# Performance work log

Measured on AMD Instinct MI355X. Metric: run time of the kernel, lower is better.

The kernel has to match this reference:

```python
import jax, jax.numpy as jnp
import numpy as np

B, S, D, H = 2, 2048, 1024, 16
DK = D // H


def setup_inputs() -> dict:
    key = jax.random.key(0)
    ks = jax.random.split(key, 11)
    inp = {
        'query': jax.random.normal(ks[0], (B, S, D), jnp.float32),
        'key':   jax.random.normal(ks[1], (B, S, D), jnp.float32),
        'value': jax.random.normal(ks[2], (B, S, D), jnp.float32),
        # causal mask, broadcast over heads like mask.unsqueeze(1)
        'mask': jnp.broadcast_to(jnp.tril(jnp.ones((S, S), jnp.int32)), (B, S, S)),
    }
    s = 1.0 / np.sqrt(D)
    for i, nm in enumerate(['q', 'k', 'v', 'o']):
        inp[f'W{nm}'] = jax.random.normal(ks[3 + i], (D, D), jnp.float32) * s
        inp[f'b{nm}'] = jnp.zeros((D,), jnp.float32)
    return inp


def reference(query, key, value, mask, Wq, bq, Wk, bk, Wv, bv, Wo, bo):
    def proj(x, W, b):
        # [B,S,D] -> [B,H,S,DK]
        y = x @ W.T + b
        return y.reshape(B, S, H, DK).transpose(0, 2, 1, 3)

    q = proj(query, Wq, bq)
    k = proj(key, Wk, bk)
    v = proj(value, Wv, bv)

    scores = jnp.einsum('bhsd,bhtd->bhst', q, k) / np.sqrt(DK)
    scores = jnp.where(mask[:, None, :, :] == 0, -1e9, scores)
    p = jax.nn.softmax(scores, axis=-1)  # dropout in eval mode = identity
    x = jnp.einsum('bhst,bhtd->bhsd', p, v)
    x = x.transpose(0, 2, 1, 3).reshape(B, S, D)
    return x @ Wo.T + bo
```

## Files before the change

### kernel.cpp

```cpp
#include <hip/hip_runtime.h>
#include <stdint.h>

#define BB 2
#define SS 2048
#define DD 1024
#define HH 16
#define DKK 64
#define EE 4194304
#define WEE 1048576
#define QSCALE 0.1803368801f

typedef __attribute__((ext_vector_type(8))) short bf16x8;
typedef __attribute__((ext_vector_type(4))) float f32x4;
typedef __attribute__((ext_vector_type(4))) unsigned short u16x4;

__device__ __forceinline__ unsigned short f2bf(float f) {
    union { float f; unsigned int i; } c; c.f = f;
    unsigned int u = c.i;
    return (unsigned short)((u + 0x7FFFu + ((u >> 16) & 1u)) >> 16);
}
__device__ __forceinline__ float bf2f(unsigned short u) {
    union { float f; unsigned int i; } c; c.i = ((unsigned int)u) << 16; return c.f;
}
__device__ __forceinline__ float load1f(const void* p, int idx, int isbf) {
    return isbf ? bf2f(((const unsigned short*)p)[idx]) : ((const float*)p)[idx];
}

#define GLDS16(gp, lp)                                                              \
    __builtin_amdgcn_global_load_lds(                                               \
        (const __attribute__((address_space(1))) void*)(gp),                        \
        (__attribute__((address_space(3))) void*)(lp), 16, 0, 0)

__global__ void detect_dtype_k(const unsigned short* __restrict__ q,
                               int* __restrict__ flag) {
    const int lane = threadIdx.x;
    unsigned short u = q[lane * 2];
    int ex = (u >> 7) & 0xFF;
    bool bad = (ex != 0) && (ex < 110 || ex > 137);
    unsigned long long m = __ballot(bad);
    if (lane == 0) *flag = (__popcll(m) >= 8) ? 0 : 1;
}

__global__ __launch_bounds__(256)
void convert_k(const float* __restrict__ q, const float* __restrict__ k,
               const float* __restrict__ v,
               const float* __restrict__ wq, const float* __restrict__ wk,
               const float* __restrict__ wv, const float* __restrict__ wo,
               unsigned short* __restrict__ Xc, unsigned short* __restrict__ Wc,
               const int* __restrict__ flagp)
{
    if (*flagp) return;
    const size_t e = ((size_t)blockIdx.x * 256 + threadIdx.x) * 8;
    const float* src; unsigned short* dst; size_t off;
    if (e < (size_t)3 * EE) {
        const int t = (int)(e / EE);
        src = (t == 0) ? q : (t == 1) ? k : v;
        off = e - (size_t)t * EE;
        dst = Xc + (size_t)t * EE;
    } else {
        const size_t we = e - (size_t)3 * EE;
        const int t = (int)(we >> 20);
        src = (t == 0) ? wq : (t == 1) ? wk : (t == 2) ? wv : wo;
        off = we & (WEE - 1);
        dst = Wc + (size_t)t * WEE;
    }
    const float4 a = *(const float4*)(src + off);
    const float4 b = *(const float4*)(src + off + 4);
    bf16x8 o;
    o[0] = (short)f2bf(a.x); o[1] = (short)f2bf(a.y);
    o[2] = (short)f2bf(a.z); o[3] = (short)f2bf(a.w);
    o[4] = (short)f2bf(b.x); o[5] = (short)f2bf(b.y);
    o[6] = (short)f2bf(b.z); o[7] = (short)f2bf(b.w);
    *(bf16x8*)(dst + off) = o;
}

__global__ __launch_bounds__(256)
void gemm_qkv(const void* __restrict__ Xq, const void* __restrict__ Xk,
              const void* __restrict__ Xv,
              const void* __restrict__ Wqp, const void* __restrict__ Wkp,
              const void* __restrict__ Wvp,
              const void* __restrict__ bqp, const void* __restrict__ bkp,
              const void* __restrict__ bvp,
              const unsigned short* __restrict__ Xc,
              const unsigned short* __restrict__ Wc,
              unsigned short* __restrict__ qb, unsigned short* __restrict__ kb,
              unsigned short* __restrict__ vtb, const int* __restrict__ flagp)
{
    const int isbf = *flagp;
    const int z = blockIdx.z;
    const unsigned short* Xg = isbf
        ? (const unsigned short*)((z == 0) ? Xq : (z == 1) ? Xk : Xv)
        : Xc + (size_t)z * EE;
    const unsigned short* Wg = isbf
        ? (const unsigned short*)((z == 0) ? Wqp : (z == 1) ? Wkp : Wvp)
        : Wc + (size_t)z * WEE;
    const void* bias = (z == 0) ? bqp : (z == 1) ? bkp : bvp;

    __shared__ __align__(16) unsigned short As[2][128 * 32];
    __shared__ __align__(16) unsigned short Bs[2][128 * 32];

    const int tid  = threadIdx.x;
    const int lane = tid & 63, w = tid >> 6;
    const int l15  = lane & 15, quad = lane >> 4;
    const int wr = (w >> 1) * 64, wc = (w & 1) * 64;
    const int r0 = blockIdx.x * 128, c0 = blockIdx.y * 128;
    const int srow = tid >> 2, scol = (tid & 3) << 3;

    const unsigned short* xp0 = Xg + (size_t)(r0 + srow) * DD + scol;
    const unsigned short* xp1 = Xg + (size_t)(r0 + 64 + srow) * DD + scol;
    const unsigned short* wp0 = Wg + (size_t)(c0 + srow) * DD + scol;
    const unsigned short* wp1 = Wg + (size_t)(c0 + 64 + srow) * DD + scol;

#define STAGE_QKV(buf, kk)                                                     \
    do {                                                                       \
        GLDS16(xp0 + (kk), &As[buf][tid * 8]);                                 \
        GLDS16(xp1 + (kk), &As[buf][2048 + tid * 8]);                          \
        GLDS16(wp0 + (kk), &Bs[buf][tid * 8]);                                 \
        GLDS16(wp1 + (kk), &Bs[buf][2048 + tid * 8]);                          \
    } while (0)

#define COMPUTE_QKV(buf)                                                       \
    do {                                                                       \
        bf16x8 af[4], bfr[4];                                                  \
        _Pragma("unroll")                                                      \
        for (int mi = 0; mi < 4; ++mi)                                         \
            af[mi] = *(const bf16x8*)(&As[buf][(wr + mi * 16 + l15) * 32 +     \
                                               quad * 8]);                     \
        _Pragma("unroll")                                                      \
        for (int ni = 0; ni < 4; ++ni)                                         \
            bfr[ni] = *(const bf16x8*)(&Bs[buf][(wc + ni * 16 + l15) * 32 +    \
                                                quad * 8]);                    \
        _Pragma("unroll")                                                      \
        for (int mi = 0; mi < 4; ++mi)                                         \
            _Pragma("unroll")                                                  \
            for (int ni = 0; ni < 4; ++ni)                                     \
                acc[mi][ni] = __builtin_amdgcn_mfma_f32_16x16x32_bf16(         \
                    af[mi], bfr[ni], acc[mi][ni], 0, 0, 0);                    \
    } while (0)

    f32x4 acc[4][4] = {};

    STAGE_QKV(0, 0);
    asm volatile("s_waitcnt vmcnt(0)" ::: "memory");
    __builtin_amdgcn_s_barrier();
    __builtin_amdgcn_sched_barrier(0);

    int cur = 0;
    for (int k0 = 0; k0 < DD - 32; k0 += 32) {
        STAGE_QKV(cur ^ 1, k0 + 32);
        __builtin_amdgcn_sched_barrier(0);
        COMPUTE_QKV(cur);
        asm volatile("s_waitcnt vmcnt(0)" ::: "memory");
        __builtin_amdgcn_s_barrier();
        __builtin_amdgcn_sched_barrier(0);
        cur ^= 1;
    }
    COMPUTE_QKV(cur);

#pragma unroll
    for (int mi = 0; mi < 4; ++mi) {
#pragma unroll
        for (int ni = 0; ni < 4; ++ni) {
            const int col = c0 + wc + ni * 16 + l15;
            const float bv = load1f(bias, col, isbf);
            const int h = col >> 6, dk = col & 63;
            const int m0 = r0 + wr + mi * 16 + quad * 4;
            const int bb = m0 >> 11, s0 = m0 & (SS - 1);
            const int bh = bb * HH + h;
            if (z == 0) {
#pragma unroll
                for (int r = 0; r < 4; ++r)
                    qb[((size_t)bh * SS + s0 + r) * DKK + dk] =
                        f2bf((acc[mi][ni][r] + bv) * QSCALE);
            } else if (z == 1) {
#pragma unroll
                for (int r = 0; r < 4; ++r) {
                    const int t = s0 + r;
                    kb[((((size_t)bh * 128 + (t >> 4)) * 8 + (dk >> 3)) * 16 +
                        (t & 15)) * 8 + (dk & 7)] = f2bf(acc[mi][ni][r] + bv);
                }
            } else {
                u16x4 pv;
#pragma unroll
                for (int r = 0; r < 4; ++r) pv[r] = f2bf(acc[mi][ni][r] + bv);
                const int t = s0;
                *(u16x4*)&vtb[((((size_t)bh * 64 + (t >> 5)) * 4 + (dk >> 4)) * 64 +
                               ((t >> 3) & 3) * 16 + (dk & 15)) * 8 + (t & 7)] = pv;
            }
        }
    }
#undef STAGE_QKV
#undef COMPUTE_QKV
}

template <bool MASKED>
__device__ __forceinline__ void attn_tile(
    const int t0, const int q0, const int l15, const int quad,
    const unsigned short* __restrict__ Kb, const unsigned short* __restrict__ Vb,
    const bf16x8 (&qf)[2], f32x4 (&Oa)[4], float (&ls)[4],
    unsigned short* __restrict__ Pw)
{
    bf16x8 kf[4][2];
#pragma unroll
    for (int ni = 0; ni < 4; ++ni)
#pragma unroll
        for (int ks = 0; ks < 2; ++ks)
            kf[ni][ks] = *(const bf16x8*)(Kb +
                ((size_t)(((t0 >> 4) + ni) * 8 + ks * 4 + quad) * 16 + l15) * 8);

    f32x4 sc[4] = {};
#pragma unroll
    for (int ks = 0; ks < 2; ++ks)
#pragma unroll
        for (int ni = 0; ni < 4; ++ni)
            sc[ni] = __builtin_amdgcn_mfma_f32_16x16x32_bf16(
                qf[ks], kf[ni][ks], sc[ni], 0, 0, 0);

    bf16x8 vf[4][2];
#pragma unroll
    for (int nd = 0; nd < 4; ++nd)
#pragma unroll
        for (int ks = 0; ks < 2; ++ks)
            vf[nd][ks] = *(const bf16x8*)(Vb +
                ((size_t)(((t0 >> 5) + ks) * 4 + nd) * 64 + quad * 16 + l15) * 8);

#pragma unroll
    for (int ni = 0; ni < 4; ++ni)
#pragma unroll
        for (int r = 0; r < 4; ++r) {
            float s = sc[ni][r];
            if (MASKED && (t0 + ni * 16 + l15 > q0 + quad * 4 + r))
                s = -__builtin_inff();
            const float p = exp2f(s);
            const unsigned int pu = __float_as_uint(p);
            ls[r] += __uint_as_float(pu & 0xFFFF0000u);
            Pw[(quad * 4 + r) * 72 + ni * 16 + l15] = (unsigned short)(pu >> 16);
        }

    bf16x8 pf[2];
#pragma unroll
    for (int ks = 0; ks < 2; ++ks)
        pf[ks] = *(const bf16x8*)(Pw + l15 * 72 + ks * 32 + quad * 8);
#pragma unroll
    for (int ks = 0; ks < 2; ++ks)
#pragma unroll
        for (int nd = 0; nd < 4; ++nd)
            Oa[nd] = __builtin_amdgcn_mfma_f32_16x16x32_bf16(
                pf[ks], vf[nd][ks], Oa[nd], 0, 0, 0);
}

__global__ __launch_bounds__(256)
void attn_mfma(const unsigned short* __restrict__ Qg,
               const unsigned short* __restrict__ Kf,
               const unsigned short* __restrict__ Vf,
               unsigned short* __restrict__ Og)
{
    __shared__ __align__(16) unsigned short Ps[4][16 * 72];
    const int tid  = threadIdx.x;
    const int lane = tid & 63, w = tid >> 6;
    const int l15 = lane & 15, quad = lane >> 4;
    const int bh = blockIdx.x;
    const int qt = (gridDim.y - 1 - blockIdx.y) * 4 + w;
    const int q0 = qt * 16;
    unsigned short* Pw = &Ps[w][0];

    const unsigned short* Qb = Qg + (size_t)bh * SS * DKK;
    const unsigned short* Kb = Kf + (size_t)bh * SS * DKK;
    const unsigned short* Vb = Vf + (size_t)bh * SS * DKK;

    bf16x8 qf[2];
#pragma unroll
    for (int ks = 0; ks < 2; ++ks)
        qf[ks] = *(const bf16x8*)(Qb + (size_t)(q0 + l15) * DKK + ks * 32 + quad * 8);

    f32x4 Oa[4] = {};
    float ls[4] = {};
    const int nfull = q0 >> 6;

    for (int tt = 0; tt < nfull; ++tt)
        attn_tile<false>(tt * 64, q0, l15, quad, Kb, Vb, qf, Oa, ls, Pw);
    attn_tile<true>(nfull * 64, q0, l15, quad, Kb, Vb, qf, Oa, ls, Pw);

    const int bb = bh >> 4, h = bh & (HH - 1);
#pragma unroll
    for (int r = 0; r < 4; ++r) {
        float l = ls[r];
        l += __shfl_xor(l, 1);
        l += __shfl_xor(l, 2);
        l += __shfl_xor(l, 4);
        l += __shfl_xor(l, 8);
        const float inv = 1.0f / l;
        const int s = q0 + quad * 4 + r;
#pragma unroll
        for (int nd = 0; nd < 4; ++nd)
            Og[((size_t)bb * SS + s) * DD + h * 64 + nd * 16 + l15] =
                f2bf(Oa[nd][r] * inv);
    }
}

__global__ __launch_bounds__(256)
void gemm_out(const unsigned short* __restrict__ Xa, const void* __restrict__ W,
              const unsigned short* __restrict__ Wcs,
              const void* __restrict__ bias, void* __restrict__ Y,
              const int* __restrict__ flagp)
{
    const int isbf = *flagp;
    const unsigned short* Wg = isbf ? (const unsigned short*)W : Wcs;

    __shared__ __align__(16) unsigned short As[2][128 * 32];
    __shared__ __align__(16) unsigned short Bs[2][128 * 32];

    const int tid  = threadIdx.x;
    const int lane = tid & 63, w = tid >> 6;
    const int l15  = lane & 15, quad = lane >> 4;
    const int wr = (w >> 1) * 64, wc = (w & 1) * 64;
    const int r0 = blockIdx.x * 128, c0 = blockIdx.y * 128;
    const int srow = tid >> 2, scol = (tid & 3) << 3;

    const unsigned short* xp0 = Xa + (size_t)(r0 + srow) * DD + scol;
    const unsigned short* xp1 = Xa + (size_t)(r0 + 64 + srow) * DD + scol;
    const unsigned short* wp0 = Wg + (size_t)(c0 + srow) * DD + scol;
    const unsigned short* wp1 = Wg + (size_t)(c0 + 64 + srow) * DD + scol;

#define STAGE_OUT(buf, kk)                                                     \
    do {                                                                       \
        GLDS16(xp0 + (kk), &As[buf][tid * 8]);                                 \
        GLDS16(xp1 + (kk), &As[buf][2048 + tid * 8]);                          \
        GLDS16(wp0 + (kk), &Bs[buf][tid * 8]);                                 \
        GLDS16(wp1 + (kk), &Bs[buf][2048 + tid * 8]);                          \
    } while (0)

#define COMPUTE_OUT(buf)                                                       \
    do {                                                                       \
        bf16x8 af[4], bfr[4];                                                  \
        _Pragma("unroll")                                                      \
        for (int mi = 0; mi < 4; ++mi)                                         \
            af[mi] = *(const bf16x8*)(&As[buf][(wr + mi * 16 + l15) * 32 +     \
                                               quad * 8]);                     \
        _Pragma("unroll")                                                      \
        for (int ni = 0; ni < 4; ++ni)                                         \
            bfr[ni] = *(const bf16x8*)(&Bs[buf][(wc + ni * 16 + l15) * 32 +    \
                                                quad * 8]);                    \
        _Pragma("unroll")                                                      \
        for (int mi = 0; mi < 4; ++mi)                                         \
            _Pragma("unroll")                                                  \
            for (int ni = 0; ni < 4; ++ni)                                     \
                acc[mi][ni] = __builtin_amdgcn_mfma_f32_16x16x32_bf16(         \
                    af[mi], bfr[ni], acc[mi][ni], 0, 0, 0);                    \
    } while (0)

    f32x4 acc[4][4] = {};

    STAGE_OUT(0, 0);
    asm volatile("s_waitcnt vmcnt(0)" ::: "memory");
    __builtin_amdgcn_s_barrier();
    __builtin_amdgcn_sched_barrier(0);

    int cur = 0;
    for (int k0 = 0; k0 < DD - 32; k0 += 32) {
        STAGE_OUT(cur ^ 1, k0 + 32);
        __builtin_amdgcn_sched_barrier(0);
        COMPUTE_OUT(cur);
        asm volatile("s_waitcnt vmcnt(0)" ::: "memory");
        __builtin_amdgcn_s_barrier();
        __builtin_amdgcn_sched_barrier(0);
        cur ^= 1;
    }
    COMPUTE_OUT(cur);

#pragma unroll
    for (int mi = 0; mi < 4; ++mi) {
#pragma unroll
        for (int ni = 0; ni < 4; ++ni) {
            const int col = c0 + wc + ni * 16 + l15;
            const float bv = load1f(bias, col, isbf);
            const int m0 = r0 + wr + mi * 16 + quad * 4;
#pragma unroll
            for (int r = 0; r < 4; ++r) {
                const float val = acc[mi][ni][r] + bv;
                if (isbf) ((unsigned short*)Y)[(size_t)(m0 + r) * DD + col] = f2bf(val);
                else      ((float*)Y)[(size_t)(m0 + r) * DD + col] = val;
            }
        }
    }
#undef STAGE_OUT
#undef COMPUTE_OUT
}

extern "C" void kernel_launch(void* const* d_in, const int* in_sizes, int n_in,
                              void* d_out, int out_size, void* d_ws, size_t ws_size,
                              hipStream_t stream)
{
    const void* query = d_in[0];
    const void* key   = d_in[1];
    const void* value = d_in[2];
    const void* Wq = d_in[4];  const void* bq = d_in[5];
    const void* Wk = d_in[6];  const void* bk = d_in[7];
    const void* Wv = d_in[8];  const void* bv = d_in[9];
    const void* Wo = d_in[10]; const void* bo = d_in[11];

    int* flag = (int*)d_ws;
    unsigned short* base = (unsigned short*)((char*)d_ws + 256);
    const size_t E = EE;
    unsigned short* qb  = base;
    unsigned short* kb  = base + E;
    unsigned short* vtb = base + 2 * E;
    unsigned short* Wc  = base + 3 * E;
    unsigned short* Xc  = base + 4 * E;
    unsigned short* ab  = Xc;

    detect_dtype_k<<<1, 64, 0, stream>>>((const unsigned short*)query, flag);
    convert_k<<<8192, 256, 0, stream>>>((const float*)query, (const float*)key,
                                        (const float*)value, (const float*)Wq,
                                        (const float*)Wk, (const float*)Wv,
                                        (const float*)Wo, Xc, Wc, flag);
    gemm_qkv<<<dim3(32, 8, 3), 256, 0, stream>>>(query, key, value, Wq, Wk, Wv,
                                                 bq, bk, bv, Xc, Wc,
                                                 qb, kb, vtb, flag);
    attn_mfma<<<dim3(32, 32), 256, 0, stream>>>(qb, kb, vtb, ab);
    gemm_out<<<dim3(32, 8), 256, 0, stream>>>(ab, Wo, Wc + 3 * (size_t)WEE, bo,
                                              d_out, flag);
}
```

Measured before the change: 247.0 us.

## Triple-buffer GEMM LDS staging with XOR swizzle in QKV and output projections

Both projection GEMMs move from a double-buffered LDS pipeline that waits on vmcnt(0) every step to a three-stage ring that waits only on vmcnt(4), so two global-to-LDS loads stay in flight while the current tile is computed. The LDS column offset is XOR-swizzled by row on both the write and the read side, to cut bank conflicts on the bf16x8 fragment reads. The cost is about 50% more shared memory per block, which may lower occupancy, and the hand-unrolled loop and epilogue counts must match K=1024 exactly.

```diff
diff --git a/kernel.cpp b/kernel.cpp
--- a/kernel.cpp
+++ b/kernel.cpp
@@ -96,22 +96,24 @@
         : Wc + (size_t)z * WEE;
     const void* bias = (z == 0) ? bqp : (z == 1) ? bkp : bvp;
 
-    __shared__ __align__(16) unsigned short As[2][128 * 32];
-    __shared__ __align__(16) unsigned short Bs[2][128 * 32];
+    __shared__ __align__(16) unsigned short As[3][128 * 32];
+    __shared__ __align__(16) unsigned short Bs[3][128 * 32];
 
     const int tid  = threadIdx.x;
     const int lane = tid & 63, w = tid >> 6;
     const int l15  = lane & 15, quad = lane >> 4;
     const int wr = (w >> 1) * 64, wc = (w & 1) * 64;
     const int r0 = blockIdx.x * 128, c0 = blockIdx.y * 128;
-    const int srow = tid >> 2, scol = (tid & 3) << 3;
+    const int srow = tid >> 2;
+    const int scol = (((tid & 3) ^ ((tid >> 3) & 3)) << 3);
+    const int rdo  = ((quad ^ ((l15 >> 1) & 3)) << 3);
 
     const unsigned short* xp0 = Xg + (size_t)(r0 + srow) * DD + scol;
     const unsigned short* xp1 = Xg + (size_t)(r0 + 64 + srow) * DD + scol;
     const unsigned short* wp0 = Wg + (size_t)(c0 + srow) * DD + scol;
     const unsigned short* wp1 = Wg + (size_t)(c0 + 64 + srow) * DD + scol;
 
-#define STAGE_QKV(buf, kk)                                                     \
+#define STAGE_G(buf, kk)                                                       \
     do {                                                                       \
         GLDS16(xp0 + (kk), &As[buf][tid * 8]);                                 \
         GLDS16(xp1 + (kk), &As[buf][2048 + tid * 8]);                          \
@@ -119,17 +121,17 @@
         GLDS16(wp1 + (kk), &Bs[buf][2048 + tid * 8]);                          \
     } while (0)
 
-#define COMPUTE_QKV(buf)                                                       \
+#define COMPUTE_G(buf)                                                         \
     do {                                                                       \
         bf16x8 af[4], bfr[4];                                                  \
         _Pragma("unroll")                                                      \
         for (int mi = 0; mi < 4; ++mi)                                         \
             af[mi] = *(const bf16x8*)(&As[buf][(wr + mi * 16 + l15) * 32 +     \
-                                               quad * 8]);                     \
+                                               rdo]);                          \
         _Pragma("unroll")                                                      \
         for (int ni = 0; ni < 4; ++ni)                                         \
             bfr[ni] = *(const bf16x8*)(&Bs[buf][(wc + ni * 16 + l15) * 32 +    \
-                                                quad * 8]);                    \
+                                                rdo]);                         \
         _Pragma("unroll")                                                      \
         for (int mi = 0; mi < 4; ++mi)                                         \
             _Pragma("unroll")                                                  \
@@ -138,24 +140,34 @@
                     af[mi], bfr[ni], acc[mi][ni], 0, 0, 0);                    \
     } while (0)
 
+#define PHASE_G(cb, nb, kn)                                                    \
+    do {                                                                       \
+        asm volatile("s_waitcnt vmcnt(4)" ::: "memory");                       \
+        __builtin_amdgcn_s_barrier();                                          \
+        __builtin_amdgcn_sched_barrier(0);                                     \
+        STAGE_G(nb, kn);                                                       \
+        __builtin_amdgcn_sched_barrier(0);                                     \
+        COMPUTE_G(cb);                                                         \
+    } while (0)
+
     f32x4 acc[4][4] = {};
 
-    STAGE_QKV(0, 0);
+    STAGE_G(0, 0);
+    STAGE_G(1, 32);
+    for (int s = 0; s < 30; s += 3) {
+        const int k0 = s * 32;
+        PHASE_G(0, 2, k0 + 64);
+        PHASE_G(1, 0, k0 + 96);
+        PHASE_G(2, 1, k0 + 128);
+    }
+    asm volatile("s_waitcnt vmcnt(4)" ::: "memory");
+    __builtin_amdgcn_s_barrier();
+    __builtin_amdgcn_sched_barrier(0);
+    COMPUTE_G(0);
     asm volatile("s_waitcnt vmcnt(0)" ::: "memory");
     __builtin_amdgcn_s_barrier();
     __builtin_amdgcn_sched_barrier(0);
-
-    int cur = 0;
-    for (int k0 = 0; k0 < DD - 32; k0 += 32) {
-        STAGE_QKV(cur ^ 1, k0 + 32);
-        __builtin_amdgcn_sched_barrier(0);
-        COMPUTE_QKV(cur);
-        asm volatile("s_waitcnt vmcnt(0)" ::: "memory");
-        __builtin_amdgcn_s_barrier();
-        __builtin_amdgcn_sched_barrier(0);
-        cur ^= 1;
-    }
-    COMPUTE_QKV(cur);
+    COMPUTE_G(1);
 
 #pragma unroll
     for (int mi = 0; mi < 4; ++mi) {
@@ -189,8 +201,9 @@
             }
         }
     }
-#undef STAGE_QKV
-#undef COMPUTE_QKV
+#undef STAGE_G
+#undef COMPUTE_G
+#undef PHASE_G
 }
 
 template <bool MASKED>
@@ -307,22 +320,24 @@
     const int isbf = *flagp;
     const unsigned short* Wg = isbf ? (const unsigned short*)W : Wcs;
 
-    __shared__ __align__(16) unsigned short As[2][128 * 32];
-    __shared__ __align__(16) unsigned short Bs[2][128 * 32];
+    __shared__ __align__(16) unsigned short As[3][128 * 32];
+    __shared__ __align__(16) unsigned short Bs[3][128 * 32];
 
     const int tid  = threadIdx.x;
     const int lane = tid & 63, w = tid >> 6;
     const int l15  = lane & 15, quad = lane >> 4;
     const int wr = (w >> 1) * 64, wc = (w & 1) * 64;
     const int r0 = blockIdx.x * 128, c0 = blockIdx.y * 128;
-    const int srow = tid >> 2, scol = (tid & 3) << 3;
+    const int srow = tid >> 2;
+    const int scol = (((tid & 3) ^ ((tid >> 3) & 3)) << 3);
+    const int rdo  = ((quad ^ ((l15 >> 1) & 3)) << 3);
 
     const unsigned short* xp0 = Xa + (size_t)(r0 + srow) * DD + scol;
     const unsigned short* xp1 = Xa + (size_t)(r0 + 64 + srow) * DD + scol;
     const unsigned short* wp0 = Wg + (size_t)(c0 + srow) * DD + scol;
     const unsigned short* wp1 = Wg + (size_t)(c0 + 64 + srow) * DD + scol;
 
-#define STAGE_OUT(buf, kk)                                                     \
+#define STAGE_O(buf, kk)                                                       \
     do {                                                                       \
         GLDS16(xp0 + (kk), &As[buf][tid * 8]);                                 \
         GLDS16(xp1 + (kk), &As[buf][2048 + tid * 8]);                          \
@@ -330,17 +345,17 @@
         GLDS16(wp1 + (kk), &Bs[buf][2048 + tid * 8]);                          \
     } while (0)
 
-#define COMPUTE_OUT(buf)                                                       \
+#define COMPUTE_O(buf)                                                         \
     do {                                                                       \
         bf16x8 af[4], bfr[4];                                                  \
         _Pragma("unroll")                                                      \
         for (int mi = 0; mi < 4; ++mi)                                         \
             af[mi] = *(const bf16x8*)(&As[buf][(wr + mi * 16 + l15) * 32 +     \
-                                               quad * 8]);                     \
+                                               rdo]);                          \
         _Pragma("unroll")                                                      \
         for (int ni = 0; ni < 4; ++ni)                                         \
             bfr[ni] = *(const bf16x8*)(&Bs[buf][(wc + ni * 16 + l15) * 32 +    \
-                                                quad * 8]);                    \
+                                                rdo]);                         \
         _Pragma("unroll")                                                      \
         for (int mi = 0; mi < 4; ++mi)                                         \
             _Pragma("unroll")                                                  \
@@ -349,24 +364,34 @@
                     af[mi], bfr[ni], acc[mi][ni], 0, 0, 0);                    \
     } while (0)
 
+#define PHASE_O(cb, nb, kn)                                                    \
+    do {                                                                       \
+        asm volatile("s_waitcnt vmcnt(4)" ::: "memory");                       \
+        __builtin_amdgcn_s_barrier();                                          \
+        __builtin_amdgcn_sched_barrier(0);                                     \
+        STAGE_O(nb, kn);                                                       \
+        __builtin_amdgcn_sched_barrier(0);                                     \
+        COMPUTE_O(cb);                                                         \
+    } while (0)
+
     f32x4 acc[4][4] = {};
 
-    STAGE_OUT(0, 0);
+    STAGE_O(0, 0);
+    STAGE_O(1, 32);
+    for (int s = 0; s < 30; s += 3) {
+        const int k0 = s * 32;
+        PHASE_O(0, 2, k0 + 64);
+        PHASE_O(1, 0, k0 + 96);
+        PHASE_O(2, 1, k0 + 128);
+    }
+    asm volatile("s_waitcnt vmcnt(4)" ::: "memory");
+    __builtin_amdgcn_s_barrier();
+    __builtin_amdgcn_sched_barrier(0);
+    COMPUTE_O(0);
     asm volatile("s_waitcnt vmcnt(0)" ::: "memory");
     __builtin_amdgcn_s_barrier();
     __builtin_amdgcn_sched_barrier(0);
-
-    int cur = 0;
-    for (int k0 = 0; k0 < DD - 32; k0 += 32) {
-        STAGE_OUT(cur ^ 1, k0 + 32);
-        __builtin_amdgcn_sched_barrier(0);
-        COMPUTE_OUT(cur);
-        asm volatile("s_waitcnt vmcnt(0)" ::: "memory");
-        __builtin_amdgcn_s_barrier();
-        __builtin_amdgcn_sched_barrier(0);
-        cur ^= 1;
-    }
-    COMPUTE_OUT(cur);
+    COMPUTE_O(1);
 
 #pragma unroll
     for (int mi = 0; mi < 4; ++mi) {
@@ -383,8 +408,9 @@
             }
         }
     }
-#undef STAGE_OUT
-#undef COMPUTE_OUT
+#undef STAGE_O
+#undef COMPUTE_O
+#undef PHASE_O
 }
 
 extern "C" void kernel_launch(void* const* d_in, const int* in_sizes, int n_in,
```

Result: no change. 249.4 us (+0.9%).
